# Performance work log

Hardware: AMD Instinct MI355X
Metric: run time of the kernel (lower is better)

## Reference

```python
import jax, jax.numpy as jnp
import numpy as np

N_NODES = 20000
IN_CH = 512
HEADS = 8
CH = 64  # hidden_layer per head
E = 320000
E_LABEL = 100000


def setup_inputs() -> dict:
    key = jax.random.key(0)
    ks = jax.random.split(key, 8)
    x = jax.random.normal(ks[0], (N_NODES, IN_CH), dtype=jnp.float32)
    edge_index = jax.random.randint(ks[1], (2, E), 0, N_NODES)
    edge_label_index = jax.random.randint(ks[2], (2, E_LABEL), 0, N_NODES)
    # GATv2Conv params (share_weights=False, bias=True)
    sc = 1.0 / np.sqrt(IN_CH)
    W_l = jax.random.normal(ks[3], (IN_CH, HEADS * CH), dtype=jnp.float32) * sc
    W_r = jax.random.normal(ks[4], (IN_CH, HEADS * CH), dtype=jnp.float32) * sc
    att = jax.random.normal(ks[5], (HEADS, CH), dtype=jnp.float32) * (1.0 / np.sqrt(CH))
    bias = jnp.zeros((HEADS * CH,), dtype=jnp.float32)
    gamma = jnp.ones((HEADS * CH,), dtype=jnp.float32)
    beta = jnp.zeros((HEADS * CH,), dtype=jnp.float32)
    return {"x": x, "edge_index": edge_index, "edge_label_index": edge_label_index,
            "W_l": W_l, "W_r": W_r, "att": att, "bias": bias,
            "gamma": gamma, "beta": beta}


def reference(x, edge_index, edge_label_index, W_l, W_r, att, bias, gamma, beta):
    N = x.shape[0]
    H, C = att.shape
    src, dst = edge_index[0], edge_index[1]
    # GATv2Conv: separate source/target linear maps
    xl = (x @ W_l).reshape(N, H, C)
    xr = (x @ W_r).reshape(N, H, C)
    # per-edge attention logits (GATv2: leaky_relu BEFORE attention vector)
    e = jax.nn.leaky_relu(xl[src] + xr[dst], negative_slope=0.2)  # [E,H,C]
    alpha = jnp.einsum('ehc,hc->eh', e, att)                      # [E,H]
    # softmax over incoming edges of each destination node
    amax = jax.ops.segment_max(alpha, dst, num_segments=N)        # [N,H]
    alpha = jnp.exp(alpha - amax[dst])
    denom = jax.ops.segment_sum(alpha, dst, num_segments=N)       # [N,H]
    alpha = alpha / (denom[dst] + 1e-16)
    # scatter-add aggregation of attended source messages
    out = jax.ops.segment_sum(alpha[:, :, None] * xl[src], dst, num_segments=N)  # [N,H,C]
    out = out.reshape(N, H * C) + bias
    # BatchNorm1d (training-mode batch stats, eps=1e-5)
    mu = out.mean(axis=0)
    var = out.var(axis=0)
    out = (out - mu) * jax.lax.rsqrt(var + 1e-5) * gamma + beta
    out = jax.nn.relu(out)  # dropout is identity in deterministic reference
    # gather + dot-product link scoring
    s = out[edge_label_index[0]]
    t = out[edge_label_index[1]]
    return jnp.sum(s * t, axis=1)  # [E_LABEL]
```

## Files before the change

### kernel.cpp

```cpp
#include <hip/hip_runtime.h>
#include <hip/hip_bf16.h>
#include <cstdint>

#define IN_CH 512
#define HC    512
#define HEADS 8
#define NPACK 1024

typedef __attribute__((ext_vector_type(8))) short bf16x8;
typedef __attribute__((ext_vector_type(8))) ushort u16x8;
typedef __attribute__((ext_vector_type(4))) float f32x4;
typedef const __attribute__((address_space(1))) uint8_t* gaddr_t;
typedef __attribute__((address_space(3))) uint8_t* laddr_t;

__device__ inline ushort f2bf(float f) {
  uint32_t u = __float_as_uint(f);
  return (ushort)((u + 0x7fffu + ((u >> 16) & 1u)) >> 16);
}
__device__ inline float bf2f(ushort u) {
  return __uint_as_float(((uint32_t)u) << 16);
}

__global__ void prep(const float* __restrict__ x, ushort* __restrict__ xb,
                     const float* __restrict__ Wl, const float* __restrict__ Wr,
                     ushort* __restrict__ bt,
                     const int* __restrict__ ei, int* __restrict__ counts,
                     const int* __restrict__ eli, int* __restrict__ counts2,
                     int n4, int E, int EL, int nbc, int nbp, int nbh) {
  const int b = blockIdx.x;
  if (b < nbc) {
    const int i = b * 256 + threadIdx.x;
    if (i < n4) {
      const float4 v = ((const float4*)x)[i];
      ushort4 o;
      o.x = f2bf(v.x); o.y = f2bf(v.y); o.z = f2bf(v.z); o.w = f2bf(v.w);
      ((ushort4*)xb)[i] = o;
    }
  } else if (b < nbc + nbp) {
    const int i = (b - nbc) * 256 + threadIdx.x;
    if (i < NPACK * IN_CH) {
      const int n = i >> 9, k = i & 511;
      const float v = (n < HC) ? Wl[(size_t)k * HC + n] : Wr[(size_t)k * HC + (n - HC)];
      bt[i] = f2bf(v);
    }
  } else if (b < nbc + nbp + nbh) {
    const int e = (b - nbc - nbp) * 256 + threadIdx.x;
    if (e < E) atomicAdd(&counts[ei[E + e]], 1);
  } else {
    const int e = (b - nbc - nbp - nbh) * 256 + threadIdx.x;
    if (e < EL) atomicAdd(&counts2[eli[e]], 1);
  }
}

__global__ __launch_bounds__(256) void gemm_mfma(
    const ushort* __restrict__ xb, const ushort* __restrict__ bt,
    ushort* __restrict__ xlb, ushort* __restrict__ xrb, int M) {
  __shared__ __align__(16) ushort As[128 * 32];
  __shared__ __align__(16) ushort Bs[128 * 32];
  const int wave = threadIdx.x >> 6, lane = threadIdx.x & 63;
  const int row0 = blockIdx.y * 128, col0 = blockIdx.x * 128;
  const int quad = lane >> 4, m16 = lane & 15;
  const int wrow = (wave >> 1) * 64, wcol = (wave & 1) * 64;
  const int srow = lane >> 2;
  const int scol = (lane & 3) * 8;
  const f32x4 zero = {0.f, 0.f, 0.f, 0.f};
  f32x4 acc[4][4];
  #pragma unroll
  for (int i = 0; i < 4; ++i)
    #pragma unroll
    for (int j = 0; j < 4; ++j) acc[i][j] = zero;

  for (int k0 = 0; k0 < IN_CH; k0 += 32) {
    #pragma unroll
    for (int c = 0; c < 2; ++c) {
      const int chunk = wave * 2 + c;
      const ushort* ga = xb + (size_t)(row0 + chunk * 16 + srow) * IN_CH + k0 + scol;
      __builtin_amdgcn_global_load_lds((gaddr_t)ga, (laddr_t)(As + chunk * 512), 16, 0, 0);
      const ushort* gb = bt + (size_t)(col0 + chunk * 16 + srow) * IN_CH + k0 + scol;
      __builtin_amdgcn_global_load_lds((gaddr_t)gb, (laddr_t)(Bs + chunk * 512), 16, 0, 0);
    }
    __syncthreads();
    bf16x8 af[4], bfr[4];
    #pragma unroll
    for (int i = 0; i < 4; ++i)
      af[i] = *(const bf16x8*)(As + (wrow + i * 16 + m16) * 32 + quad * 8);
    #pragma unroll
    for (int j = 0; j < 4; ++j)
      bfr[j] = *(const bf16x8*)(Bs + (wcol + j * 16 + m16) * 32 + quad * 8);
    #pragma unroll
    for (int i = 0; i < 4; ++i)
      #pragma unroll
      for (int j = 0; j < 4; ++j)
        acc[i][j] = __builtin_amdgcn_mfma_f32_16x16x32_bf16(af[i], bfr[j], acc[i][j], 0, 0, 0);
    __syncthreads();
  }
  const bool isL = (col0 < HC);
  ushort* dst = isL ? xlb : xrb;
  const int cbase = isL ? col0 : (col0 - HC);
  #pragma unroll
  for (int i = 0; i < 4; ++i) {
    const int r = row0 + wrow + i * 16 + quad * 4;
    #pragma unroll
    for (int j = 0; j < 4; ++j) {
      const int cg = cbase + wcol + j * 16 + m16;
      #pragma unroll
      for (int t = 0; t < 4; ++t) {
        const int rr = r + t;
        if (rr < M) dst[(size_t)rr * HC + cg] = f2bf(acc[i][j][t]);
      }
    }
  }
}

__global__ void scan1(const int* __restrict__ cA, int* __restrict__ oA, int* __restrict__ bA,
                      const int* __restrict__ cB, int* __restrict__ oB, int* __restrict__ bB,
                      int Nn, int nb) {
  const int half = (blockIdx.x >= nb) ? 1 : 0;
  const int blk  = blockIdx.x - half * nb;
  const int* counts = half ? cB : cA;
  int* offsets = half ? oB : oA;
  int* bsums   = half ? bB : bA;
  __shared__ int tmp[256];
  const int t = threadIdx.x;
  const int i = blk * 256 + t;
  const int v = (i < Nn) ? counts[i] : 0;
  tmp[t] = v;
  __syncthreads();
  for (int d = 1; d < 256; d <<= 1) {
    int add = (t >= d) ? tmp[t - d] : 0;
    __syncthreads();
    tmp[t] += add;
    __syncthreads();
  }
  if (i < Nn) offsets[i] = tmp[t] - v;
  if (t == 255) bsums[blk] = tmp[255];
}

__global__ void scan3(int* __restrict__ oA, const int* __restrict__ bA, int* __restrict__ curA,
                      int* __restrict__ oB, const int* __restrict__ bB, int* __restrict__ curB,
                      int Nn, int nb) {
  const int half = (blockIdx.x >= nb) ? 1 : 0;
  const int blk  = blockIdx.x - half * nb;
  int* offsets = half ? oB : oA;
  const int* bsums = half ? bB : bA;
  int* cursor  = half ? curB : curA;
  __shared__ int pref;
  if (threadIdx.x < 64) {
    int s = 0;
    for (int b = threadIdx.x; b < blk; b += 64) s += bsums[b];
    #pragma unroll
    for (int off = 32; off > 0; off >>= 1) s += __shfl_down(s, off, 64);
    if (threadIdx.x == 0) pref = s;
  }
  __syncthreads();
  const int i = blk * 256 + threadIdx.x;
  if (i < Nn) {
    const int o = offsets[i] + pref;
    offsets[i] = o;
    cursor[i] = o;
  }
}

__global__ void csr_fill(const int* __restrict__ ei, int* __restrict__ cursor,
                         int* __restrict__ csr_src,
                         const int* __restrict__ eli, int* __restrict__ cursor2,
                         int* __restrict__ csr_t, int* __restrict__ csr_eid,
                         int E, int EL, int nbE) {
  const int b = blockIdx.x;
  if (b < nbE) {
    const int e = b * 256 + threadIdx.x;
    if (e < E) {
      const int pos = atomicAdd(&cursor[ei[E + e]], 1);
      csr_src[pos] = ei[e];
    }
  } else {
    const int e = (b - nbE) * 256 + threadIdx.x;
    if (e < EL) {
      const int pos = atomicAdd(&cursor2[eli[e]], 1);
      csr_t[pos] = eli[EL + e];
      csr_eid[pos] = e;
    }
  }
}

__global__ __launch_bounds__(256) void gatv2_agg(
    const ushort* __restrict__ xlb, const ushort* xrb, const float* __restrict__ att,
    const int* __restrict__ offsets, const int* __restrict__ counts,
    const int* __restrict__ csr_src, ushort* agg, int Nn) {
  const int node = blockIdx.x * 4 + (threadIdx.x >> 6);
  const int lane = threadIdx.x & 63;
  if (node >= Nn) return;
  const int start = offsets[node];
  const int deg   = counts[node];
  float rv[8], tv[8];
  {
    const u16x8 ur = *(const u16x8*)(xrb + (size_t)node * HC + lane * 8);
    #pragma unroll
    for (int c = 0; c < 8; ++c) rv[c] = bf2f((ushort)ur[c]);
    const float4* pa = (const float4*)(att + lane * 8);
    const float4 t0 = pa[0], t1 = pa[1];
    tv[0]=t0.x; tv[1]=t0.y; tv[2]=t0.z; tv[3]=t0.w;
    tv[4]=t1.x; tv[5]=t1.y; tv[6]=t1.z; tv[7]=t1.w;
  }
  float acc[8] = {};
  float densum = 0.f;
  const int* ps = csr_src + start;
  auto row = [&](int idx) {
    return *(const u16x8*)(xlb + (size_t)ps[idx] * HC + lane * 8);
  };
  auto body = [&](const u16x8 cur) {
    float a[8];
    #pragma unroll
    for (int c = 0; c < 8; ++c) a[c] = bf2f((ushort)cur[c]);
    float s = 0.f;
    #pragma unroll
    for (int c = 0; c < 8; ++c) {
      const float v = a[c] + rv[c];
      s += fmaxf(v, 0.2f * v) * tv[c];
    }
    s += __shfl_xor(s, 1, 8);
    s += __shfl_xor(s, 2, 8);
    s += __shfl_xor(s, 4, 8);
    const float ea = __expf(s);
    densum += ea;
    #pragma unroll
    for (int c = 0; c < 8; ++c) acc[c] += ea * a[c];
  };

  u16x8 b0 = {}, b1 = {};
  if (deg > 0) b0 = row(0);
  if (deg > 1) b1 = row(1);
  int i = 0;
  for (; i + 2 <= deg; i += 2) {
    const u16x8 c0 = b0;
    if (i + 2 < deg) b0 = row(i + 2);
    const u16x8 c1 = b1;
    if (i + 3 < deg) b1 = row(i + 3);
    body(c0);
    body(c1);
  }
  if (i < deg) body(b0);

  const float inv = 1.0f / (densum + 1e-16f);
  ushort* pd = agg + (size_t)node * HC + lane * 8;
  ushort4 o0, o1;
  o0.x = f2bf(acc[0] * inv); o0.y = f2bf(acc[1] * inv);
  o0.z = f2bf(acc[2] * inv); o0.w = f2bf(acc[3] * inv);
  o1.x = f2bf(acc[4] * inv); o1.y = f2bf(acc[5] * inv);
  o1.z = f2bf(acc[6] * inv); o1.w = f2bf(acc[7] * inv);
  *(ushort4*)(pd + 0) = o0;
  *(ushort4*)(pd + 4) = o1;
}

__global__ void bn_stats(const ushort* __restrict__ agg, float* __restrict__ gsum,
                         float* __restrict__ gsq, int Nn) {
  const int t = threadIdx.x;
  const int rows_per_block = (Nn + gridDim.x - 1) / gridDim.x;
  const int r0 = blockIdx.x * rows_per_block;
  const int r1 = min(Nn, r0 + rows_per_block);
  float s0 = 0.f, s1 = 0.f, q0 = 0.f, q1 = 0.f;
  for (int r = r0; r < r1; ++r) {
    const ushort2 u = ((const ushort2*)(agg + (size_t)r * HC))[t];
    const float v0 = bf2f(u.x), v1 = bf2f(u.y);
    s0 += v0; q0 += v0 * v0;
    s1 += v1; q1 += v1 * v1;
  }
  atomicAdd(&gsum[2 * t], s0);
  atomicAdd(&gsum[2 * t + 1], s1);
  atomicAdd(&gsq[2 * t], q0);
  atomicAdd(&gsq[2 * t + 1], q1);
}

__global__ void bn_apply(const ushort* __restrict__ agg, const float* __restrict__ gsum,
                         const float* __restrict__ gsq, const float* __restrict__ gamma,
                         const float* __restrict__ beta, ushort* __restrict__ y,
                         float invN, int total4) {
  const int i = blockIdx.x * blockDim.x + threadIdx.x;
  if (i >= total4) return;
  const int base = i << 2;
  const int c = base & (HC - 1);
  const float4 gs = *(const float4*)(gsum + c);
  const float4 gq = *(const float4*)(gsq + c);
  const float4 ga = *(const float4*)(gamma + c);
  const float4 be = *(const float4*)(beta + c);
  const ushort4 u = *(const ushort4*)(agg + base);
  float m, var;
  ushort4 o;
  m = gs.x * invN; var = gq.x * invN - m * m;
  o.x = f2bf(fmaxf(0.f, (bf2f(u.x) - m) * rsqrtf(var + 1e-5f) * ga.x + be.x));
  m = gs.y * invN; var = gq.y * invN - m * m;
  o.y = f2bf(fmaxf(0.f, (bf2f(u.y) - m) * rsqrtf(var + 1e-5f) * ga.y + be.y));
  m = gs.z * invN; var = gq.z * invN - m * m;
  o.z = f2bf(fmaxf(0.f, (bf2f(u.z) - m) * rsqrtf(var + 1e-5f) * ga.z + be.z));
  m = gs.w * invN; var = gq.w * invN - m * m;
  o.w = f2bf(fmaxf(0.f, (bf2f(u.w) - m) * rsqrtf(var + 1e-5f) * ga.w + be.w));
  *(ushort4*)(y + base) = o;
}

__global__ __launch_bounds__(256) void score_g(
    const ushort* __restrict__ y, const int* __restrict__ off2,
    const int* __restrict__ cnt2, const int* __restrict__ csr_t,
    const int* __restrict__ csr_eid, float* __restrict__ out, int Nn) {
  const int node = blockIdx.x * 4 + (threadIdx.x >> 6);
  const int lane = threadIdx.x & 63;
  if (node >= Nn) return;
  const int start = off2[node];
  const int deg   = cnt2[node];
  if (deg == 0) return;
  float a[8];
  {
    const u16x8 us = *(const u16x8*)(y + (size_t)node * HC + lane * 8);
    #pragma unroll
    for (int c = 0; c < 8; ++c) a[c] = bf2f((ushort)us[c]);
  }
  const int* pt = csr_t + start;
  const int* pe = csr_eid + start;
  auto row = [&](int idx) {
    return *(const u16x8*)(y + (size_t)pt[idx] * HC + lane * 8);
  };
  auto emit = [&](const u16x8 ut, int eid) {
    float s = 0.f;
    #pragma unroll
    for (int c = 0; c < 8; ++c) s += a[c] * bf2f((ushort)ut[c]);
    #pragma unroll
    for (int off = 32; off > 0; off >>= 1) s += __shfl_down(s, off, 64);
    if (lane == 0) out[eid] = s;
  };
  u16x8 b0 = {}, b1 = {};
  b0 = row(0);
  if (deg > 1) b1 = row(1);
  int j = 0;
  for (; j + 2 <= deg; j += 2) {
    const u16x8 c0 = b0;
    if (j + 2 < deg) b0 = row(j + 2);
    const u16x8 c1 = b1;
    if (j + 3 < deg) b1 = row(j + 3);
    emit(c0, pe[j]);
    emit(c1, pe[j + 1]);
  }
  if (j < deg) emit(b0, pe[j]);
}

extern "C" void kernel_launch(void* const* d_in, const int* in_sizes, int n_in,
                              void* d_out, int out_size, void* d_ws, size_t ws_size,
                              hipStream_t stream) {
  const float* x     = (const float*)d_in[0];
  const int*   ei    = (const int*)d_in[1];
  const int*   eli   = (const int*)d_in[2];
  const float* W_l   = (const float*)d_in[3];
  const float* W_r   = (const float*)d_in[4];
  const float* att   = (const float*)d_in[5];
  const float* gamma = (const float*)d_in[7];
  const float* beta  = (const float*)d_in[8];
  float* out = (float*)d_out;

  const int Nn = in_sizes[0] / IN_CH;
  const int E  = in_sizes[1] / 2;
  const int EL = in_sizes[2] / 2;

  ushort* xlb = (ushort*)d_ws;
  ushort* xrb = xlb + (size_t)Nn * HC;
  ushort* xbf = xrb + (size_t)Nn * HC;
  ushort* btb = xbf + (size_t)Nn * IN_CH;
  int* counts   = (int*)(btb + (size_t)NPACK * IN_CH);
  int* counts2  = counts + Nn;
  float* gsum   = (float*)(counts2 + Nn);
  float* gsq    = gsum + HC;
  int* offsets  = (int*)(gsq + HC);
  int* cursor   = offsets + Nn;
  int* bsumsA   = cursor + Nn;
  int* offsets2 = bsumsA + 256;
  int* cursor2  = offsets2 + Nn;
  int* bsumsB   = cursor2 + Nn;
  int* csr_src  = bsumsB + 256;
  int* csr_t    = csr_src + E;
  int* csr_eid  = csr_t + EL;
  ushort* agg = xrb;
  ushort* y   = xlb;

  const int nb  = (Nn + 255) / 256;
  const int nbc = (Nn * IN_CH / 4 + 255) / 256;
  const int nbp = (NPACK * IN_CH + 255) / 256;
  const int nbh = (E + 255) / 256;
  const int nbh2 = (EL + 255) / 256;

  hipMemsetAsync(counts, 0, (2 * (size_t)Nn + 2 * HC) * sizeof(int), stream);

  prep<<<nbc + nbp + nbh + nbh2, 256, 0, stream>>>(
      x, xbf, W_l, W_r, btb, ei, counts, eli, counts2,
      Nn * IN_CH / 4, E, EL, nbc, nbp, nbh);

  dim3 ggrid(NPACK / 128, (Nn + 127) / 128);
  gemm_mfma<<<ggrid, 256, 0, stream>>>(xbf, btb, xlb, xrb, Nn);

  scan1<<<2 * nb, 256, 0, stream>>>(counts, offsets, bsumsA,
                                    counts2, offsets2, bsumsB, Nn, nb);
  scan3<<<2 * nb, 256, 0, stream>>>(offsets, bsumsA, cursor,
                                    offsets2, bsumsB, cursor2, Nn, nb);
  csr_fill<<<nbh + nbh2, 256, 0, stream>>>(ei, cursor, csr_src,
                                           eli, cursor2, csr_t, csr_eid, E, EL, nbh);

  gatv2_agg<<<(Nn + 3) / 4, 256, 0, stream>>>(xlb, xrb, att, offsets, counts,
                                              csr_src, agg, Nn);

  bn_stats<<<200, 256, 0, stream>>>(agg, gsum, gsq, Nn);
  bn_apply<<<(Nn * HC / 4 + 255) / 256, 256, 0, stream>>>(
      agg, gsum, gsq, gamma, beta, y, 1.0f / (float)Nn, Nn * HC / 4);

  score_g<<<(Nn + 3) / 4, 256, 0, stream>>>(y, offsets2, counts2, csr_t, csr_eid,
                                            out, Nn);
}
```

Before: 303.3 us.

## Fuse scan passes with decoupled lookback and fold BatchNorm apply into scoring

Merges the two-pass prefix scan into a single kernel in which each block publishes its sum through flags and spin-waits on the flags of earlier blocks. Drops the separate BatchNorm apply pass: the last stats block computes per-channel scale and shift, and the scoring kernel applies the affine transform and ReLU on the fly to the rows it gathers. This removes two launches plus a full read and write of the N×512 activation buffer, at the cost of redundant normalization math per gathered row. The spin-wait relies on earlier blocks being scheduled first, which holds for only 158 blocks.

```diff
diff --git a/kernel.cpp b/kernel.cpp
--- a/kernel.cpp
+++ b/kernel.cpp
@@ -112,15 +112,19 @@
   }
 }
 
-__global__ void scan1(const int* __restrict__ cA, int* __restrict__ oA, int* __restrict__ bA,
-                      const int* __restrict__ cB, int* __restrict__ oB, int* __restrict__ bB,
-                      int Nn, int nb) {
+__global__ __launch_bounds__(256) void scan_fused(
+    const int* __restrict__ cA, int* __restrict__ oA, int* __restrict__ curA,
+    int* __restrict__ fA,
+    const int* __restrict__ cB, int* __restrict__ oB, int* __restrict__ curB,
+    int* __restrict__ fB, int Nn, int nb) {
   const int half = (blockIdx.x >= nb) ? 1 : 0;
   const int blk  = blockIdx.x - half * nb;
   const int* counts = half ? cB : cA;
   int* offsets = half ? oB : oA;
-  int* bsums   = half ? bB : bA;
+  int* cursor  = half ? curB : curA;
+  int* flags   = half ? fB : fA;
   __shared__ int tmp[256];
+  __shared__ int sPref;
   const int t = threadIdx.x;
   const int i = blk * 256 + t;
   const int v = (i < Nn) ? counts[i] : 0;
@@ -132,30 +136,22 @@
     tmp[t] += add;
     __syncthreads();
   }
-  if (i < Nn) offsets[i] = tmp[t] - v;
-  if (t == 255) bsums[blk] = tmp[255];
-}
-
-__global__ void scan3(int* __restrict__ oA, const int* __restrict__ bA, int* __restrict__ curA,
-                      int* __restrict__ oB, const int* __restrict__ bB, int* __restrict__ curB,
-                      int Nn, int nb) {
-  const int half = (blockIdx.x >= nb) ? 1 : 0;
-  const int blk  = blockIdx.x - half * nb;
-  int* offsets = half ? oB : oA;
-  const int* bsums = half ? bB : bA;
-  int* cursor  = half ? curB : curA;
-  __shared__ int pref;
-  if (threadIdx.x < 64) {
+  if (t == 0) atomicExch(&flags[blk], tmp[255] + 1);
+  if (t < 64) {
     int s = 0;
-    for (int b = threadIdx.x; b < blk; b += 64) s += bsums[b];
+    for (int b = t; b < blk; b += 64) {
+      int f;
+      do { f = atomicOr(&flags[b], 0); } while (f == 0);
+      s += f - 1;
+    }
     #pragma unroll
     for (int off = 32; off > 0; off >>= 1) s += __shfl_down(s, off, 64);
-    if (threadIdx.x == 0) pref = s;
+    if (t == 0) sPref = s;
   }
   __syncthreads();
-  const int i = blk * 256 + threadIdx.x;
+  const int pref = sPref;
   if (i < Nn) {
-    const int o = offsets[i] + pref;
+    const int o = tmp[t] - v + pref;
     offsets[i] = o;
     cursor[i] = o;
   }
@@ -253,7 +249,10 @@
 }
 
 __global__ void bn_stats(const ushort* __restrict__ agg, float* __restrict__ gsum,
-                         float* __restrict__ gsq, int Nn) {
+                         float* __restrict__ gsq, int* __restrict__ ctr,
+                         const float* __restrict__ gamma, const float* __restrict__ beta,
+                         float* __restrict__ aScale, float* __restrict__ bShift,
+                         float invN, int Nn) {
   const int t = threadIdx.x;
   const int rows_per_block = (Nn + gridDim.x - 1) / gridDim.x;
   const int r0 = blockIdx.x * rows_per_block;
@@ -269,36 +268,32 @@
   atomicAdd(&gsum[2 * t + 1], s1);
   atomicAdd(&gsq[2 * t], q0);
   atomicAdd(&gsq[2 * t + 1], q1);
-}
-
-__global__ void bn_apply(const ushort* __restrict__ agg, const float* __restrict__ gsum,
-                         const float* __restrict__ gsq, const float* __restrict__ gamma,
-                         const float* __restrict__ beta, ushort* __restrict__ y,
-                         float invN, int total4) {
-  const int i = blockIdx.x * blockDim.x + threadIdx.x;
-  if (i >= total4) return;
-  const int base = i << 2;
-  const int c = base & (HC - 1);
-  const float4 gs = *(const float4*)(gsum + c);
-  const float4 gq = *(const float4*)(gsq + c);
-  const float4 ga = *(const float4*)(gamma + c);
-  const float4 be = *(const float4*)(beta + c);
-  const ushort4 u = *(const ushort4*)(agg + base);
-  float m, var;
-  ushort4 o;
-  m = gs.x * invN; var = gq.x * invN - m * m;
-  o.x = f2bf(fmaxf(0.f, (bf2f(u.x) - m) * rsqrtf(var + 1e-5f) * ga.x + be.x));
-  m = gs.y * invN; var = gq.y * invN - m * m;
-  o.y = f2bf(fmaxf(0.f, (bf2f(u.y) - m) * rsqrtf(var + 1e-5f) * ga.y + be.y));
-  m = gs.z * invN; var = gq.z * invN - m * m;
-  o.z = f2bf(fmaxf(0.f, (bf2f(u.z) - m) * rsqrtf(var + 1e-5f) * ga.z + be.z));
-  m = gs.w * invN; var = gq.w * invN - m * m;
-  o.w = f2bf(fmaxf(0.f, (bf2f(u.w) - m) * rsqrtf(var + 1e-5f) * ga.w + be.w));
-  *(ushort4*)(y + base) = o;
+  __shared__ int isLast;
+  __syncthreads();
+  if (t == 0) {
+    __threadfence();
+    isLast = (atomicAdd(ctr, 1) == (int)gridDim.x - 1) ? 1 : 0;
+  }
+  __syncthreads();
+  if (isLast) {
+    #pragma unroll
+    for (int k = 0; k < 2; ++k) {
+      const int c = t + k * 256;
+      const float sum = atomicAdd(&gsum[c], 0.0f);
+      const float sq  = atomicAdd(&gsq[c], 0.0f);
+      const float m = sum * invN;
+      const float var = sq * invN - m * m;
+      const float rs = rsqrtf(var + 1e-5f);
+      const float a = rs * gamma[c];
+      aScale[c] = a;
+      bShift[c] = beta[c] - m * a;
+    }
+  }
 }
 
 __global__ __launch_bounds__(256) void score_g(
-    const ushort* __restrict__ y, const int* __restrict__ off2,
+    const ushort* __restrict__ agg, const float* __restrict__ aScale,
+    const float* __restrict__ bShift, const int* __restrict__ off2,
     const int* __restrict__ cnt2, const int* __restrict__ csr_t,
     const int* __restrict__ csr_eid, float* __restrict__ out, int Nn) {
   const int node = blockIdx.x * 4 + (threadIdx.x >> 6);
@@ -307,21 +302,31 @@
   const int start = off2[node];
   const int deg   = cnt2[node];
   if (deg == 0) return;
-  float a[8];
+  float aS[8], bS[8], ys[8];
   {
-    const u16x8 us = *(const u16x8*)(y + (size_t)node * HC + lane * 8);
-    #pragma unroll
-    for (int c = 0; c < 8; ++c) a[c] = bf2f((ushort)us[c]);
+    const float4* pa = (const float4*)(aScale + lane * 8);
+    const float4 a0 = pa[0], a1 = pa[1];
+    aS[0]=a0.x; aS[1]=a0.y; aS[2]=a0.z; aS[3]=a0.w;
+    aS[4]=a1.x; aS[5]=a1.y; aS[6]=a1.z; aS[7]=a1.w;
+    const float4* pb = (const float4*)(bShift + lane * 8);
+    const float4 c0 = pb[0], c1 = pb[1];
+    bS[0]=c0.x; bS[1]=c0.y; bS[2]=c0.z; bS[3]=c0.w;
+    bS[4]=c1.x; bS[5]=c1.y; bS[6]=c1.z; bS[7]=c1.w;
+    const u16x8 us = *(const u16x8*)(agg + (size_t)node * HC + lane * 8);
+    #pragma unroll
+    for (int c = 0; c < 8; ++c)
+      ys[c] = fmaxf(0.f, bf2f((ushort)us[c]) * aS[c] + bS[c]);
   }
   const int* pt = csr_t + start;
   const int* pe = csr_eid + start;
   auto row = [&](int idx) {
-    return *(const u16x8*)(y + (size_t)pt[idx] * HC + lane * 8);
+    return *(const u16x8*)(agg + (size_t)pt[idx] * HC + lane * 8);
   };
   auto emit = [&](const u16x8 ut, int eid) {
     float s = 0.f;
     #pragma unroll
-    for (int c = 0; c < 8; ++c) s += a[c] * bf2f((ushort)ut[c]);
+    for (int c = 0; c < 8; ++c)
+      s += ys[c] * fmaxf(0.f, bf2f((ushort)ut[c]) * aS[c] + bS[c]);
     #pragma unroll
     for (int off = 32; off > 0; off >>= 1) s += __shfl_down(s, off, 64);
     if (lane == 0) out[eid] = s;
@@ -366,17 +371,19 @@
   int* counts2  = counts + Nn;
   float* gsum   = (float*)(counts2 + Nn);
   float* gsq    = gsum + HC;
-  int* offsets  = (int*)(gsq + HC);
+  int* flagsA   = (int*)(gsq + HC);
+  int* flagsB   = flagsA + 128;
+  int* bnctr    = flagsB + 128;
+  int* offsets  = bnctr + 64;
   int* cursor   = offsets + Nn;
-  int* bsumsA   = cursor + Nn;
-  int* offsets2 = bsumsA + 256;
+  int* offsets2 = cursor + Nn;
   int* cursor2  = offsets2 + Nn;
-  int* bsumsB   = cursor2 + Nn;
-  int* csr_src  = bsumsB + 256;
+  int* csr_src  = cursor2 + Nn;
   int* csr_t    = csr_src + E;
   int* csr_eid  = csr_t + EL;
+  float* aScale = (float*)(csr_eid + EL);
+  float* bShift = aScale + HC;
   ushort* agg = xrb;
-  ushort* y   = xlb;
 
   const int nb  = (Nn + 255) / 256;
   const int nbc = (Nn * IN_CH / 4 + 255) / 256;
@@ -384,7 +391,7 @@
   const int nbh = (E + 255) / 256;
   const int nbh2 = (EL + 255) / 256;
 
-  hipMemsetAsync(counts, 0, (2 * (size_t)Nn + 2 * HC) * sizeof(int), stream);
+  (void)hipMemsetAsync(counts, 0, (2 * (size_t)Nn + 2 * HC + 320) * sizeof(int), stream);
 
   prep<<<nbc + nbp + nbh + nbh2, 256, 0, stream>>>(
       x, xbf, W_l, W_r, btb, ei, counts, eli, counts2,
@@ -393,20 +400,17 @@
   dim3 ggrid(NPACK / 128, (Nn + 127) / 128);
   gemm_mfma<<<ggrid, 256, 0, stream>>>(xbf, btb, xlb, xrb, Nn);
 
-  scan1<<<2 * nb, 256, 0, stream>>>(counts, offsets, bsumsA,
-                                    counts2, offsets2, bsumsB, Nn, nb);
-  scan3<<<2 * nb, 256, 0, stream>>>(offsets, bsumsA, cursor,
-                                    offsets2, bsumsB, cursor2, Nn, nb);
+  scan_fused<<<2 * nb, 256, 0, stream>>>(counts, offsets, cursor, flagsA,
+                                         counts2, offsets2, cursor2, flagsB, Nn, nb);
   csr_fill<<<nbh + nbh2, 256, 0, stream>>>(ei, cursor, csr_src,
                                            eli, cursor2, csr_t, csr_eid, E, EL, nbh);
 
   gatv2_agg<<<(Nn + 3) / 4, 256, 0, stream>>>(xlb, xrb, att, offsets, counts,
                                               csr_src, agg, Nn);
 
-  bn_stats<<<200, 256, 0, stream>>>(agg, gsum, gsq, Nn);
-  bn_apply<<<(Nn * HC / 4 + 255) / 256, 256, 0, stream>>>(
-      agg, gsum, gsq, gamma, beta, y, 1.0f / (float)Nn, Nn * HC / 4);
-
-  score_g<<<(Nn + 3) / 4, 256, 0, stream>>>(y, offsets2, counts2, csr_t, csr_eid,
-                                            out, Nn);
-}
+  bn_stats<<<200, 256, 0, stream>>>(agg, gsum, gsq, bnctr, gamma, beta,
+                                    aScale, bShift, 1.0f / (float)Nn, Nn);
+
+  score_g<<<(Nn + 3) / 4, 256, 0, stream>>>(agg, aScale, bShift, offsets2,
+                                            counts2, csr_t, csr_eid, out, Nn);
+}
```

New measurement: 297.8 us (median of 2 runs). No clear change (-1.8%).
